# Performance work log

Hardware: AMD Instinct MI355X
Metric: run time of the kernel (lower is better)

The kernel has to match this reference:

```python
import jax, jax.numpy as jnp
import numpy as np

B = 8192
ID_DIM = 1024
LLM_DIM = 4096
IN_DIM = ID_DIM + LLM_DIM      # 5120
OUT_DIM = 2048
HID = OUT_DIM * 2              # 4096
E = 8
TOPK = 2
GATE_HID = E * 2               # 16


def setup_inputs() -> dict:
    key = jax.random.key(0)
    ks = jax.random.split(key, 12)
    s_in = 1.0 / np.sqrt(IN_DIM)
    s_hid = 1.0 / np.sqrt(HID)
    s_g = 1.0 / np.sqrt(GATE_HID)
    return {
        "id_emb": jax.random.normal(ks[0], (B, ID_DIM), jnp.float32),
        "llm_emb": jax.random.normal(ks[1], (B, LLM_DIM), jnp.float32),
        # stacked expert params
        "W1": jax.random.normal(ks[2], (E, IN_DIM, HID), jnp.float32) * s_in,
        "b1": jax.random.normal(ks[3], (E, HID), jnp.float32) * 0.01,
        "W2": jax.random.normal(ks[4], (E, HID, OUT_DIM), jnp.float32) * s_hid,
        "b2": jax.random.normal(ks[5], (E, OUT_DIM), jnp.float32) * 0.01,
        # gate params
        "gW1": jax.random.normal(ks[6], (IN_DIM, GATE_HID), jnp.float32) * s_in,
        "gb1": jax.random.normal(ks[7], (GATE_HID,), jnp.float32) * 0.01,
        "gW2": jax.random.normal(ks[8], (GATE_HID, E), jnp.float32) * s_g,
        "gb2": jax.random.normal(ks[9], (E,), jnp.float32) * 0.01,
    }


def reference(id_emb, llm_emb, W1, b1, W2, b2, gW1, gb1, gW2, gb2):
    combined = jnp.concatenate([id_emb, llm_emb], axis=-1)          # [B, IN]
    # gate: Linear -> ReLU -> Linear
    gate_logits = jax.nn.relu(combined @ gW1 + gb1) @ gW2 + gb2    # [B, E]
    topk_w, topk_i = jax.lax.top_k(gate_logits, TOPK)               # [B, K]
    topk_w = jax.nn.softmax(topk_w, axis=-1)
    # dense per-expert combine weights [B, E] (zero for non-selected experts)
    bsz = combined.shape[0]
    dense_w = jnp.zeros((bsz, E), combined.dtype).at[
        jnp.arange(bsz)[:, None], topk_i].add(topk_w)
    # dense all-experts MLP (faithful to reference: every expert on all tokens)
    h = jax.nn.relu(jnp.einsum('bi,eih->beh', combined, W1) + b1)  # [B, E, HID]
    expert_out = jnp.einsum('beh,eho->beo', h, W2) + b2            # [B, E, OUT]
    return jnp.einsum('be,beo->bo', dense_w, expert_out)           # [B, OUT]
```

## Files before the change

kernel.cpp:

```cpp
#include <hip/hip_runtime.h>
#include <hip/hip_bf16.h>
#include <hip/hip_fp16.h>

#define B_TOK 8192
#define ID_DIM 1024
#define LLM_DIM 4096
#define IN_DIM 5120
#define OUT_DIM 2048
#define HID 4096
#define NE 8
#define GH 16
#define NSLOT (2 * B_TOK)

#define NNT1 16
#define NKS1 160
#define NNT2 8
#define NKS2 128
#define MT256 72
#define GRID1B (MT256 * NNT1)
#define GRID2B (MT256 * NNT2)

typedef _Float16 f16x8 __attribute__((ext_vector_type(8)));
typedef float f32x4 __attribute__((ext_vector_type(4)));
typedef unsigned short u16;
typedef u16 u16x8 __attribute__((ext_vector_type(8)));

#define OFF_H   (1ull << 20)
#define OFF_X   (OFF_H + (size_t)NSLOT * HID * 2)
#define OFF_P1  (OFF_X + (size_t)B_TOK * IN_DIM * 2)
#define OFF_P2  (OFF_P1 + (size_t)NE * NNT1 * NKS1 * 16384)
#define REQ_WS  (OFF_P2 + (size_t)NE * NNT2 * NKS2 * 16384)
#define OFF_SLOT OFF_P1

#define INV_OFF 66560

__device__ __forceinline__ void gll16(void* lds, const void* gsrc) {
  __builtin_amdgcn_global_load_lds(
      (const __attribute__((address_space(1))) unsigned int*)gsrc,
      (__attribute__((address_space(3))) unsigned int*)lds, 16, 0, 0);
}

__global__ __launch_bounds__(256) void gate_kernel(
    const float* __restrict__ id_emb, const float* __restrict__ llm_emb,
    const float* __restrict__ gW1, const float* __restrict__ gb1,
    const float* __restrict__ gW2, const float* __restrict__ gb2,
    int* __restrict__ wsi, _Float16* __restrict__ xf16) {
  int wave = (blockIdx.x * blockDim.x + threadIdx.x) >> 6;
  int lane = threadIdx.x & 63;
  if (wave >= B_TOK) return;
  int b = wave;
  float acc[GH];
#pragma unroll
  for (int j = 0; j < GH; ++j) acc[j] = 0.f;
  for (int k = lane; k < IN_DIM; k += 64) {
    float x = (k < ID_DIM) ? id_emb[(size_t)b * ID_DIM + k]
                           : llm_emb[(size_t)b * LLM_DIM + (k - ID_DIM)];
    if (xf16) xf16[(size_t)b * IN_DIM + k] = (_Float16)x;
    const float* grow = gW1 + (size_t)k * GH;
#pragma unroll
    for (int j = 0; j < GH; ++j) acc[j] += x * grow[j];
  }
#pragma unroll
  for (int j = 0; j < GH; ++j) {
    for (int off = 32; off > 0; off >>= 1) acc[j] += __shfl_xor(acc[j], off);
  }
  if (lane == 0) {
    float logits[NE];
#pragma unroll
    for (int e = 0; e < NE; ++e) logits[e] = gb2[e];
#pragma unroll
    for (int j = 0; j < GH; ++j) {
      float hg = fmaxf(acc[j] + gb1[j], 0.f);
#pragma unroll
      for (int e = 0; e < NE; ++e) logits[e] += hg * gW2[j * NE + e];
    }
    int i0 = 0; float v0 = logits[0];
#pragma unroll
    for (int e = 1; e < NE; ++e) if (logits[e] > v0) { v0 = logits[e]; i0 = e; }
    int i1 = -1; float v1 = -1e30f;
#pragma unroll
    for (int e = 0; e < NE; ++e) if (e != i0 && logits[e] > v1) { v1 = logits[e]; i1 = e; }
    float ex = expf(v1 - v0);
    float w0 = 1.f / (1.f + ex);
    float w1 = ex / (1.f + ex);
    int* eidx = wsi + 1024;
    float* wsl = (float*)(wsi + 17408);
    eidx[b * 2] = i0; eidx[b * 2 + 1] = i1;
    wsl[b * 2] = w0; wsl[b * 2 + 1] = w1;
    atomicAdd(&wsi[i0], 1);
    atomicAdd(&wsi[i1], 1);
  }
}

__global__ void schedule_kernel(int* __restrict__ wsi) {
  if (threadIdx.x != 0 || blockIdx.x != 0) return;
  int* counts = wsi; int* cursor = wsi + 8;
  int* te = wsi + 16; int* tm = wsi + 272; int* tc = wsi + 528;
  int off = 0, t = 0;
  for (int e = 0; e < NE; ++e) {
    int c = counts[e];
    cursor[e] = off;
    int nt = (c + 255) >> 8;
    for (int i = 0; i < nt; ++i) {
      te[t] = e; tm[t] = off + i * 256;
      int rem = c - i * 256;
      tc[t] = rem < 256 ? rem : 256;
      ++t;
    }
    off += c;
  }
  for (; t < MT256; ++t) { te[t] = 0; tm[t] = 0; tc[t] = 0; }
}

__global__ __launch_bounds__(256) void scatter_kernel(int* __restrict__ wsi) {
  int s = blockIdx.x * blockDim.x + threadIdx.x;
  if (s >= NSLOT) return;
  int* cursor = wsi + 8;
  const int* eidx = wsi + 1024;
  const float* wsl = (const float*)(wsi + 17408);
  int* rows = wsi + 33792;
  float* wsorted = (float*)(wsi + 50176);
  int* inv = wsi + INV_OFF;
  int e = eidx[s];
  int pos = atomicAdd(&cursor[e], 1);
  rows[pos] = s;
  wsorted[pos] = wsl[s];
  inv[s] = pos;
}

__global__ __launch_bounds__(256) void pack_w(
    const float* __restrict__ W, _Float16* __restrict__ P,
    int N, int NNT, int NKS) {
  int ks = blockIdx.x, nt = blockIdx.y, e = blockIdx.z;
  const float* src = W + ((size_t)e * NKS * 32 + (size_t)ks * 32) * N + nt * 256;
  _Float16* dst = P + (((size_t)e * NNT + nt) * NKS + ks) * 8192;
  int t = threadIdx.x;
  int l = t & 63, q = t >> 6;
  int fr = l & 15, kg = l >> 4;
  for (int gn = q; gn < 16; gn += 4) {
    const float* s = src + (size_t)(kg * 8) * N + gn * 16 + fr;
    union { u16x8 u; _Float16 f[8]; } cv;
#pragma unroll
    for (int j = 0; j < 8; ++j) cv.f[j] = (_Float16)s[(size_t)j * N];
    *(u16x8*)(dst + gn * 512 + l * 8) = cv.u;
  }
}

#define SBAR __builtin_amdgcn_s_barrier()
#define SCHB __builtin_amdgcn_sched_barrier(0)
#define LGKM0 asm volatile("s_waitcnt lgkmcnt(0)" ::: "memory")
#define VMW(n) asm volatile("s_waitcnt vmcnt(" #n ")" ::: "memory")

#define ST_A(Aw, ks_, pa_, gm_) gll16((Aw) + (gm_) * 512, (pa_) + (size_t)(ks_) * 32)
#define ST_B(Bw, ks_, gn_) \
  gll16((Bw) + (gn_) * 512, pb + (size_t)(ks_) * 8192 + (gn_) * 512)

#define GEMM_LOOP(NKS)                                                         \
  {                                                                            \
    _Pragma("unroll") for (int kp = 0; kp < 3; ++kp) {                         \
      _Float16* Aw = smem + kp * 8192;                                         \
      _Float16* Bw = smem + 32768 + kp * 8192;                                 \
      ST_A(Aw, kp, paA, gm_a); ST_A(Aw, kp, paB, gm_b);                        \
      ST_B(Bw, kp, gnA); ST_B(Bw, kp, gnB);                                    \
    }                                                                          \
    VMW(8); SCHB; SBAR;                                                        \
    for (int k = 0; k < (NKS); ++k) {                                          \
      int rb = k & 3, wbi = (k + 3) & 3;                                       \
      _Float16* Ac = smem + rb * 8192;                                         \
      _Float16* Bc = smem + 32768 + rb * 8192;                                 \
      _Float16* Aw = smem + wbi * 8192;                                        \
      _Float16* Bw = smem + 32768 + wbi * 8192;                                \
      f16x8 a[4], b4[4];                                                       \
                                          \
      _Pragma("unroll") for (int m = 0; m < 4; ++m)                            \
          a[m] = *(const f16x8*)(Ac + (wr * 8 + m) * 512 + lane * 8);          \
      _Pragma("unroll") for (int n = 0; n < 4; ++n)                            \
          b4[n] = *(const f16x8*)(Bc + (wc * 4 + n) * 512 + lane * 8);         \
      if (k + 3 < (NKS)) {                                                     \
        ST_A(Aw, k + 3, paA, gm_a); ST_A(Aw, k + 3, paB, gm_b);                \
        ST_B(Bw, k + 3, gnA); ST_B(Bw, k + 3, gnB);                            \
      }                                                                        \
      SBAR; LGKM0; SCHB;                                                       \
      __builtin_amdgcn_s_setprio(1);                                           \
      _Pragma("unroll") for (int m = 0; m < 4; ++m)                            \
          _Pragma("unroll") for (int n = 0; n < 4; ++n)                        \
              acc[m][n] = __builtin_amdgcn_mfma_f32_16x16x32_f16(              \
                  a[m], b4[n], acc[m][n], 0, 0, 0);                            \
      __builtin_amdgcn_s_setprio(0); SCHB; SBAR;                               \
                          \
      _Pragma("unroll") for (int m = 0; m < 4; ++m)                            \
          a[m] = *(const f16x8*)(Ac + (wr * 8 + 4 + m) * 512 + lane * 8);      \
      if (k < (NKS) - 3) { VMW(8); }                                           \
      else if (k == (NKS) - 3) { VMW(4); }                                     \
      else if (k == (NKS) - 2) { VMW(0); }                                     \
      SCHB; SBAR; LGKM0; SCHB;                                                 \
      __builtin_amdgcn_s_setprio(1);                                           \
      _Pragma("unroll") for (int m = 0; m < 4; ++m)                            \
          _Pragma("unroll") for (int n = 0; n < 4; ++n)                        \
              acc[4 + m][n] = __builtin_amdgcn_mfma_f32_16x16x32_f16(          \
                  a[m], b4[n], acc[4 + m][n], 0, 0, 0);                        \
      __builtin_amdgcn_s_setprio(0); SCHB; SBAR;                               \
    }                                                                          \
  }

__global__ __launch_bounds__(512, 2) void gemm1_kernel(
    const _Float16* __restrict__ Xf, const _Float16* __restrict__ P1,
    const float* __restrict__ b1, const int* __restrict__ wsi,
    _Float16* __restrict__ hbuf) {
  __shared__ _Float16 smem[65536];
  int d = blockIdx.x;
  int orig = (d & 7) * (GRID1B >> 3) + (d >> 3);
  int tile = orig / NNT1;
  int nt = orig % NNT1;
  int cnt = (wsi + 528)[tile];
  if (cnt == 0) return;
  int e = (wsi + 16)[tile];
  int m0 = (wsi + 272)[tile];
  const int* rows = wsi + 33792;
  int n0 = nt * 256;
  int tid = threadIdx.x, lane = tid & 63, w = tid >> 6;
  int wr = w >> 2, wc = w & 3;
  int fr = lane & 15, kg = lane >> 4;

  int gm_a = wr * 8 + (w & 3);
  int gm_b = gm_a + 4;
  int gnA = w * 2, gnB = w * 2 + 1;
  int ra = gm_a * 16 + fr; ra = ra < cnt ? ra : cnt - 1;
  int rb2 = gm_b * 16 + fr; rb2 = rb2 < cnt ? rb2 : cnt - 1;
  const _Float16* paA = Xf + (size_t)(rows[m0 + ra] >> 1) * IN_DIM + kg * 8;
  const _Float16* paB = Xf + (size_t)(rows[m0 + rb2] >> 1) * IN_DIM + kg * 8;
  const _Float16* pb = P1 + ((size_t)e * NNT1 + nt) * ((size_t)NKS1 * 8192) + lane * 8;

  f32x4 acc[8][4];
#pragma unroll
  for (int m = 0; m < 8; ++m)
#pragma unroll
    for (int n = 0; n < 4; ++n) acc[m][n] = (f32x4){0.f, 0.f, 0.f, 0.f};

  GEMM_LOOP(NKS1)

  float bias_n[4];
#pragma unroll
  for (int n = 0; n < 4; ++n) bias_n[n] = b1[e * HID + n0 + wc * 64 + n * 16 + fr];

  _Float16* ep = smem;
#pragma unroll
  for (int hh = 0; hh < 2; ++hh) {
    __syncthreads();
    if (wr == hh) {
#pragma unroll
      for (int m = 0; m < 8; ++m)
#pragma unroll
        for (int n = 0; n < 4; ++n)
#pragma unroll
          for (int r2 = 0; r2 < 4; ++r2) {
            int row_loc = m * 16 + kg * 4 + r2;
            int col_loc = wc * 64 + n * 16 + fr;
            ep[row_loc * 264 + col_loc] = (_Float16)fmaxf(acc[m][n][r2] + bias_n[n], 0.f);
          }
    }
    __syncthreads();
#pragma unroll
    for (int i = 0; i < 8; ++i) {
      int chunk = i * 512 + tid;
      int row = chunk >> 5, c16 = chunk & 31;
      int r = hh * 128 + row;
      if (r < cnt)
        *(u16x8*)&hbuf[(size_t)(m0 + r) * HID + n0 + c16 * 8] =
            *(const u16x8*)&ep[row * 264 + c16 * 8];
    }
  }
}

__global__ __launch_bounds__(512, 2) void gemm2_kernel(
    const _Float16* __restrict__ hbuf, const _Float16* __restrict__ P2,
    const float* __restrict__ b2, const int* __restrict__ wsi,
    float* __restrict__ slotbuf) {
  __shared__ _Float16 smem[65536];
  int d = blockIdx.x;
  int orig = (d & 7) * (GRID2B >> 3) + (d >> 3);
  int tile = orig / NNT2;
  int nt = orig % NNT2;
  int cnt = (wsi + 528)[tile];
  if (cnt == 0) return;
  int e = (wsi + 16)[tile];
  int m0 = (wsi + 272)[tile];
  const float* wsorted = (const float*)(wsi + 50176);
  int n0 = nt * 256;
  int tid = threadIdx.x, lane = tid & 63, w = tid >> 6;
  int wr = w >> 2, wc = w & 3;
  int fr = lane & 15, kg = lane >> 4;

  int gm_a = wr * 8 + (w & 3);
  int gm_b = gm_a + 4;
  int gnA = w * 2, gnB = w * 2 + 1;
  int ra = gm_a * 16 + fr; ra = ra < cnt ? ra : cnt - 1;
  int rb2 = gm_b * 16 + fr; rb2 = rb2 < cnt ? rb2 : cnt - 1;
  const _Float16* paA = hbuf + (size_t)(m0 + ra) * HID + kg * 8;
  const _Float16* paB = hbuf + (size_t)(m0 + rb2) * HID + kg * 8;
  const _Float16* pb = P2 + ((size_t)e * NNT2 + nt) * ((size_t)NKS2 * 8192) + lane * 8;

  f32x4 acc[8][4];
#pragma unroll
  for (int m = 0; m < 8; ++m)
#pragma unroll
    for (int n = 0; n < 4; ++n) acc[m][n] = (f32x4){0.f, 0.f, 0.f, 0.f};

  GEMM_LOOP(NKS2)

  float bias_n[4];
#pragma unroll
  for (int n = 0; n < 4; ++n) bias_n[n] = b2[e * OUT_DIM + n0 + wc * 64 + n * 16 + fr];

#pragma unroll
  for (int m = 0; m < 8; ++m) {
#pragma unroll
    for (int r2 = 0; r2 < 4; ++r2) {
      int r = wr * 128 + m * 16 + kg * 4 + r2;
      if (r < cnt) {
        float wgt = wsorted[m0 + r];
        float* orow = slotbuf + (size_t)(m0 + r) * OUT_DIM + n0;
#pragma unroll
        for (int n = 0; n < 4; ++n)
          orow[wc * 64 + n * 16 + fr] = (acc[m][n][r2] + bias_n[n]) * wgt;
      }
    }
  }
}

__global__ __launch_bounds__(256) void combine_kernel(
    const float* __restrict__ slotbuf, const int* __restrict__ wsi,
    float* __restrict__ out) {
  int idx = blockIdx.x * 256 + threadIdx.x;
  int b = idx >> 9, c4 = (idx & 511) * 4;
  const int* inv = wsi + INV_OFF;
  int p0 = inv[b * 2], p1 = inv[b * 2 + 1];
  float4 a = *(const float4*)&slotbuf[(size_t)p0 * OUT_DIM + c4];
  float4 c = *(const float4*)&slotbuf[(size_t)p1 * OUT_DIM + c4];
  float4 o; o.x = a.x + c.x; o.y = a.y + c.y; o.z = a.z + c.z; o.w = a.w + c.w;
  *(float4*)&out[(size_t)b * OUT_DIM + c4] = o;
}

#define FB_MAX_TILES 136
__global__ void schedule_fb(int* __restrict__ wsi) {
  if (threadIdx.x != 0 || blockIdx.x != 0) return;
  int* counts = wsi; int* cursor = wsi + 8;
  int* te = wsi + 16; int* tm = wsi + 272; int* tc = wsi + 528;
  int off = 0, t = 0;
  for (int e = 0; e < NE; ++e) {
    int c = counts[e];
    cursor[e] = off;
    int nt = (c + 127) >> 7;
    for (int i = 0; i < nt; ++i) {
      te[t] = e; tm[t] = off + i * 128;
      int rem = c - i * 128;
      tc[t] = rem < 128 ? rem : 128;
      ++t;
    }
    off += c;
  }
  for (; t < FB_MAX_TILES; ++t) { te[t] = 0; tm[t] = 0; tc[t] = 0; }
}

__global__ __launch_bounds__(256, 2) void gemm1_fb(
    const float* __restrict__ id_emb, const float* __restrict__ llm_emb,
    const float* __restrict__ W1, const float* __restrict__ b1,
    const int* __restrict__ wsi, _Float16* __restrict__ h) {
  const int* te = wsi + 16; const int* tm = wsi + 272; const int* tc = wsi + 528;
  const int* rows = wsi + 33792;
  int tile = blockIdx.x;
  int cnt = tc[tile];
  if (cnt == 0) return;
  int e = te[tile], m0 = tm[tile];
  int n0 = blockIdx.y * 128;
  const float* Wb = W1 + (size_t)e * IN_DIM * HID;
  __shared__ _Float16 As[128][40];
  __shared__ _Float16 Bs[128][40];
  int tid = threadIdx.x;
  int lane = tid & 63, w = tid >> 6;
  int wr = w >> 1, wc = w & 1;
  int fr = lane & 15, kg = lane >> 4;
  f32x4 acc[4][4];
#pragma unroll
  for (int m = 0; m < 4; ++m)
#pragma unroll
    for (int n = 0; n < 4; ++n) acc[m][n] = (f32x4){0.f, 0.f, 0.f, 0.f};
  int a_ks = (tid & 3) * 8;
  int a_r = tid >> 2;
  int brow[2];
#pragma unroll
  for (int i = 0; i < 2; ++i) {
    int r = a_r + i * 64;
    brow[i] = (r < cnt) ? (rows[m0 + r] >> 1) : -1;
  }
  int b_c = tid & 127, b_kq = tid >> 7;
  for (int kt = 0; kt < IN_DIM; kt += 32) {
#pragma unroll
    for (int i = 0; i < 2; ++i) {
      int r = a_r + i * 64;
      float v[8];
      if (brow[i] >= 0) {
        int k = kt + a_ks;
        const float* src = (k < ID_DIM)
            ? (id_emb + (size_t)brow[i] * ID_DIM + k)
            : (llm_emb + (size_t)brow[i] * LLM_DIM + (k - ID_DIM));
        float4 v0 = *(const float4*)src;
        float4 v1 = *(const float4*)(src + 4);
        v[0] = v0.x; v[1] = v0.y; v[2] = v0.z; v[3] = v0.w;
        v[4] = v1.x; v[5] = v1.y; v[6] = v1.z; v[7] = v1.w;
      } else {
#pragma unroll
        for (int j = 0; j < 8; ++j) v[j] = 0.f;
      }
      union { u16x8 u; _Float16 f[8]; } cv;
#pragma unroll
      for (int j = 0; j < 8; ++j) cv.f[j] = (_Float16)v[j];
      *reinterpret_cast<u16x8*>(&As[r][a_ks]) = cv.u;
    }
#pragma unroll
    for (int i = 0; i < 2; ++i) {
      int kc = b_kq + i * 2;
      int k0 = kt + kc * 8;
      union { u16x8 u; _Float16 f[8]; } cv;
#pragma unroll
      for (int j = 0; j < 8; ++j)
        cv.f[j] = (_Float16)Wb[(size_t)(k0 + j) * HID + n0 + b_c];
      *reinterpret_cast<u16x8*>(&Bs[b_c][kc * 8]) = cv.u;
    }
    __syncthreads();
    f16x8 af[4], bf[4];
#pragma unroll
    for (int m = 0; m < 4; ++m)
      af[m] = *reinterpret_cast<const f16x8*>(&As[wr * 64 + m * 16 + fr][kg * 8]);
#pragma unroll
    for (int n = 0; n < 4; ++n)
      bf[n] = *reinterpret_cast<const f16x8*>(&Bs[wc * 64 + n * 16 + fr][kg * 8]);
#pragma unroll
    for (int m = 0; m < 4; ++m)
#pragma unroll
      for (int n = 0; n < 4; ++n)
        acc[m][n] = __builtin_amdgcn_mfma_f32_16x16x32_f16(af[m], bf[n], acc[m][n], 0, 0, 0);
    __syncthreads();
  }
#pragma unroll
  for (int m = 0; m < 4; ++m) {
    int rbv = wr * 64 + m * 16 + kg * 4;
#pragma unroll
    for (int n = 0; n < 4; ++n) {
      int col = n0 + wc * 64 + n * 16 + fr;
      float bias = b1[e * HID + col];
#pragma unroll
      for (int r2 = 0; r2 < 4; ++r2) {
        int r = rbv + r2;
        if (r < cnt) {
          float v = fmaxf(acc[m][n][r2] + bias, 0.f);
          h[(size_t)(m0 + r) * HID + col] = (_Float16)v;
        }
      }
    }
  }
}

__global__ __launch_bounds__(256, 2) void gemm2_fb(
    const _Float16* __restrict__ h, const float* __restrict__ W2,
    const float* __restrict__ b2, const int* __restrict__ wsi,
    float* __restrict__ out) {
  const int* te = wsi + 16; const int* tm = wsi + 272; const int* tc = wsi + 528;
  const int* rows = wsi + 33792;
  const float* wsorted = (const float*)(wsi + 50176);
  int tile = blockIdx.x;
  int cnt = tc[tile];
  if (cnt == 0) return;
  int e = te[tile], m0 = tm[tile];
  int n0 = blockIdx.y * 128;
  const float* Wb = W2 + (size_t)e * HID * OUT_DIM;
  __shared__ _Float16 As[128][40];
  __shared__ _Float16 Bs[128][40];
  int tid = threadIdx.x;
  int lane = tid & 63, w = tid >> 6;
  int wr = w >> 1, wc = w & 1;
  int fr = lane & 15, kg = lane >> 4;
  f32x4 acc[4][4];
#pragma unroll
  for (int m = 0; m < 4; ++m)
#pragma unroll
    for (int n = 0; n < 4; ++n) acc[m][n] = (f32x4){0.f, 0.f, 0.f, 0.f};
  int a_ks = (tid & 3) * 8;
  int a_r = tid >> 2;
  int b_c = tid & 127, b_kq = tid >> 7;
  for (int kt = 0; kt < HID; kt += 32) {
#pragma unroll
    for (int i = 0; i < 2; ++i) {
      int r = a_r + i * 64;
      u16x8 v;
      if (r < cnt) {
        v = *reinterpret_cast<const u16x8*>(&h[(size_t)(m0 + r) * HID + kt + a_ks]);
      } else {
        v = (u16x8){0, 0, 0, 0, 0, 0, 0, 0};
      }
      *reinterpret_cast<u16x8*>(&As[r][a_ks]) = v;
    }
#pragma unroll
    for (int i = 0; i < 2; ++i) {
      int kc = b_kq + i * 2;
      int k0 = kt + kc * 8;
      union { u16x8 u; _Float16 f[8]; } cv;
#pragma unroll
      for (int j = 0; j < 8; ++j)
        cv.f[j] = (_Float16)Wb[(size_t)(k0 + j) * OUT_DIM + n0 + b_c];
      *reinterpret_cast<u16x8*>(&Bs[b_c][kc * 8]) = cv.u;
    }
    __syncthreads();
    f16x8 af[4], bf[4];
#pragma unroll
    for (int m = 0; m < 4; ++m)
      af[m] = *reinterpret_cast<const f16x8*>(&As[wr * 64 + m * 16 + fr][kg * 8]);
#pragma unroll
    for (int n = 0; n < 4; ++n)
      bf[n] = *reinterpret_cast<const f16x8*>(&Bs[wc * 64 + n * 16 + fr][kg * 8]);
#pragma unroll
    for (int m = 0; m < 4; ++m)
#pragma unroll
      for (int n = 0; n < 4; ++n)
        acc[m][n] = __builtin_amdgcn_mfma_f32_16x16x32_f16(af[m], bf[n], acc[m][n], 0, 0, 0);
    __syncthreads();
  }
#pragma unroll
  for (int m = 0; m < 4; ++m) {
    int rbv = wr * 64 + m * 16 + kg * 4;
#pragma unroll
    for (int n = 0; n < 4; ++n) {
      int col = n0 + wc * 64 + n * 16 + fr;
      float bias = b2[e * OUT_DIM + col];
#pragma unroll
      for (int r2 = 0; r2 < 4; ++r2) {
        int r = rbv + r2;
        if (r < cnt) {
          int slot = rows[m0 + r];
          int btok = slot >> 1;
          float wgt = wsorted[m0 + r];
          atomicAdd(&out[(size_t)btok * OUT_DIM + col], (acc[m][n][r2] + bias) * wgt);
        }
      }
    }
  }
}

extern "C" void kernel_launch(void* const* d_in, const int* in_sizes, int n_in,
                              void* d_out, int out_size, void* d_ws, size_t ws_size,
                              hipStream_t stream) {
  const float* id_emb  = (const float*)d_in[0];
  const float* llm_emb = (const float*)d_in[1];
  const float* W1  = (const float*)d_in[2];
  const float* b1  = (const float*)d_in[3];
  const float* W2  = (const float*)d_in[4];
  const float* b2  = (const float*)d_in[5];
  const float* gW1 = (const float*)d_in[6];
  const float* gb1 = (const float*)d_in[7];
  const float* gW2 = (const float*)d_in[8];
  const float* gb2 = (const float*)d_in[9];
  float* out = (float*)d_out;
  int* wsi = (int*)d_ws;
  _Float16* h = (_Float16*)((char*)d_ws + OFF_H);
  bool fast = ws_size >= REQ_WS;

  hipMemsetAsync(d_ws, 0, 4096, stream);

  if (fast) {
    _Float16* xf = (_Float16*)((char*)d_ws + OFF_X);
    _Float16* p1 = (_Float16*)((char*)d_ws + OFF_P1);
    _Float16* p2 = (_Float16*)((char*)d_ws + OFF_P2);
    float* slotbuf = (float*)((char*)d_ws + OFF_SLOT);
    gate_kernel<<<B_TOK / 4, 256, 0, stream>>>(id_emb, llm_emb, gW1, gb1, gW2, gb2, wsi, xf);
    schedule_kernel<<<1, 64, 0, stream>>>(wsi);
    scatter_kernel<<<NSLOT / 256, 256, 0, stream>>>(wsi);
    pack_w<<<dim3(NKS1, NNT1, NE), 256, 0, stream>>>(W1, p1, HID, NNT1, NKS1);
    pack_w<<<dim3(NKS2, NNT2, NE), 256, 0, stream>>>(W2, p2, OUT_DIM, NNT2, NKS2);
    gemm1_kernel<<<GRID1B, 512, 0, stream>>>(xf, p1, b1, wsi, h);
    gemm2_kernel<<<GRID2B, 512, 0, stream>>>(h, p2, b2, wsi, slotbuf);
    combine_kernel<<<(B_TOK * OUT_DIM / 4) / 256, 256, 0, stream>>>(slotbuf, wsi, out);
  } else {
    hipMemsetAsync(d_out, 0, (size_t)B_TOK * OUT_DIM * sizeof(float), stream);
    gate_kernel<<<B_TOK / 4, 256, 0, stream>>>(id_emb, llm_emb, gW1, gb1, gW2, gb2, wsi, nullptr);
    schedule_fb<<<1, 64, 0, stream>>>(wsi);
    scatter_kernel<<<NSLOT / 256, 256, 0, stream>>>(wsi);
    gemm1_fb<<<dim3(FB_MAX_TILES, 32), 256, 0, stream>>>(id_emb, llm_emb, W1, b1, wsi, h);
    gemm2_fb<<<dim3(FB_MAX_TILES, 16), 256, 0, stream>>>(h, W2, b2, wsi, out);
  }
}
```

Measured before the change: 1.933 ms.

## Software-pipeline LDS fragment reads across k-steps with register double buffering

Replaces the GEMM main loop with a two-way unrolled pipeline. The next k-step's A0/B fragments are read from LDS while the current MFMAs issue, using ping-pong register sets. This cuts the loop from four barriers and two explicit lgkmcnt waits per k-step to one barrier. The goal is to hide LDS read latency behind MFMA work. It costs more VGPRs at 2 blocks per CU, and the single barrier means the 4-buffer ring must still prevent overwriting a stage that other waves are reading.

After: 1.856 ms. 1.04x faster.

```diff
diff --git a/kernel.cpp b/kernel.cpp
--- a/kernel.cpp
+++ b/kernel.cpp
@@ -148,59 +148,59 @@
 
 #define SBAR __builtin_amdgcn_s_barrier()
 #define SCHB __builtin_amdgcn_sched_barrier(0)
-#define LGKM0 asm volatile("s_waitcnt lgkmcnt(0)" ::: "memory")
 #define VMW(n) asm volatile("s_waitcnt vmcnt(" #n ")" ::: "memory")
 
 #define ST_A(Aw, ks_, pa_, gm_) gll16((Aw) + (gm_) * 512, (pa_) + (size_t)(ks_) * 32)
 #define ST_B(Bw, ks_, gn_) \
   gll16((Bw) + (gn_) * 512, pb + (size_t)(ks_) * 8192 + (gn_) * 512)
 
-#define GEMM_LOOP(NKS)                                                         \
-  {                                                                            \
-    _Pragma("unroll") for (int kp = 0; kp < 3; ++kp) {                         \
-      _Float16* Aw = smem + kp * 8192;                                         \
-      _Float16* Bw = smem + 32768 + kp * 8192;                                 \
-      ST_A(Aw, kp, paA, gm_a); ST_A(Aw, kp, paB, gm_b);                        \
-      ST_B(Bw, kp, gnA); ST_B(Bw, kp, gnB);                                    \
-    }                                                                          \
-    VMW(8); SCHB; SBAR;                                                        \
-    for (int k = 0; k < (NKS); ++k) {                                          \
-      int rb = k & 3, wbi = (k + 3) & 3;                                       \
-      _Float16* Ac = smem + rb * 8192;                                         \
-      _Float16* Bc = smem + 32768 + rb * 8192;                                 \
-      _Float16* Aw = smem + wbi * 8192;                                        \
-      _Float16* Bw = smem + 32768 + wbi * 8192;                                \
-      f16x8 a[4], b4[4];                                                       \
-                                          \
-      _Pragma("unroll") for (int m = 0; m < 4; ++m)                            \
-          a[m] = *(const f16x8*)(Ac + (wr * 8 + m) * 512 + lane * 8);          \
-      _Pragma("unroll") for (int n = 0; n < 4; ++n)                            \
-          b4[n] = *(const f16x8*)(Bc + (wc * 4 + n) * 512 + lane * 8);         \
-      if (k + 3 < (NKS)) {                                                     \
-        ST_A(Aw, k + 3, paA, gm_a); ST_A(Aw, k + 3, paB, gm_b);                \
-        ST_B(Bw, k + 3, gnA); ST_B(Bw, k + 3, gnB);                            \
-      }                                                                        \
-      SBAR; LGKM0; SCHB;                                                       \
-      __builtin_amdgcn_s_setprio(1);                                           \
-      _Pragma("unroll") for (int m = 0; m < 4; ++m)                            \
-          _Pragma("unroll") for (int n = 0; n < 4; ++n)                        \
-              acc[m][n] = __builtin_amdgcn_mfma_f32_16x16x32_f16(              \
-                  a[m], b4[n], acc[m][n], 0, 0, 0);                            \
-      __builtin_amdgcn_s_setprio(0); SCHB; SBAR;                               \
-                          \
-      _Pragma("unroll") for (int m = 0; m < 4; ++m)                            \
-          a[m] = *(const f16x8*)(Ac + (wr * 8 + 4 + m) * 512 + lane * 8);      \
-      if (k < (NKS) - 3) { VMW(8); }                                           \
-      else if (k == (NKS) - 3) { VMW(4); }                                     \
-      else if (k == (NKS) - 2) { VMW(0); }                                     \
-      SCHB; SBAR; LGKM0; SCHB;                                                 \
-      __builtin_amdgcn_s_setprio(1);                                           \
-      _Pragma("unroll") for (int m = 0; m < 4; ++m)                            \
-          _Pragma("unroll") for (int n = 0; n < 4; ++n)                        \
-              acc[4 + m][n] = __builtin_amdgcn_mfma_f32_16x16x32_f16(          \
-                  a[m], b4[n], acc[4 + m][n], 0, 0, 0);                        \
-      __builtin_amdgcn_s_setprio(0); SCHB; SBAR;                               \
-    }                                                                          \
+#define STAGE4(kt)                                                   \
+  { _Float16* Aw = smem + ((kt) & 3) * 8192;                         \
+    _Float16* Bw = smem + 32768 + ((kt) & 3) * 8192;                 \
+    ST_A(Aw, kt, paA, gm_a); ST_A(Aw, kt, paB, gm_b);                \
+    ST_B(Bw, kt, gnA); ST_B(Bw, kt, gnB); }
+
+#define READ_A0B(A0s, Bs, Acp, Bcp)                                   \
+  _Pragma("unroll") for (int m = 0; m < 4; ++m)                       \
+      A0s[m] = *(const f16x8*)((Acp) + (wr * 8 + m) * 512 + lane * 8);\
+  _Pragma("unroll") for (int n = 0; n < 4; ++n)                       \
+      Bs[n] = *(const f16x8*)((Bcp) + (wc * 4 + n) * 512 + lane * 8);
+
+#define READ_A1(Acp)                                                  \
+  _Pragma("unroll") for (int m = 0; m < 4; ++m)                       \
+      A1[m] = *(const f16x8*)((Acp) + (wr * 8 + 4 + m) * 512 + lane * 8);
+
+#define MFMA_CL(As, Bs, MO)                                           \
+  __builtin_amdgcn_s_setprio(1);                                      \
+  _Pragma("unroll") for (int m = 0; m < 4; ++m)                       \
+      _Pragma("unroll") for (int n = 0; n < 4; ++n)                   \
+          acc[(MO) + m][n] = __builtin_amdgcn_mfma_f32_16x16x32_f16(  \
+              As[m], Bs[n], acc[(MO) + m][n], 0, 0, 0);               \
+  __builtin_amdgcn_s_setprio(0);
+
+#define PIPE_ITER(A0c, Bc_, A0n, Bn_, k, NKS)                         \
+  { if ((k) < (NKS) - 2) { VMW(4); } else { VMW(0); }                 \
+    SCHB; SBAR;                                                       \
+    if ((k) + 3 < (NKS)) STAGE4((k) + 3);                             \
+    _Float16* Acur = smem + ((k) & 3) * 8192;                         \
+    READ_A1(Acur); SCHB;                                              \
+    MFMA_CL(A0c, Bc_, 0)                                              \
+    if ((k) + 1 < (NKS)) {                                            \
+      _Float16* An_ = smem + (((k) + 1) & 3) * 8192;                  \
+      _Float16* Bn2 = smem + 32768 + (((k) + 1) & 3) * 8192;          \
+      READ_A0B(A0n, Bn_, An_, Bn2)                                    \
+    }                                                                 \
+    SCHB;                                                             \
+    MFMA_CL(A1, Bc_, 4) }
+
+#define GEMM_PIPE(NKS)                                                \
+  f16x8 A0x[4], Bx[4], A0y[4], By[4], A1[4];                          \
+  STAGE4(0) STAGE4(1) STAGE4(2)                                       \
+  VMW(8); SCHB; SBAR;                                                 \
+  READ_A0B(A0x, Bx, smem, smem + 32768)                               \
+  for (int k = 0; k < (NKS); k += 2) {                                \
+    PIPE_ITER(A0x, Bx, A0y, By, k, (NKS))                             \
+    PIPE_ITER(A0y, By, A0x, Bx, (k + 1), (NKS))                       \
   }
 
 __global__ __launch_bounds__(512, 2) void gemm1_kernel(
@@ -237,7 +237,7 @@
 #pragma unroll
     for (int n = 0; n < 4; ++n) acc[m][n] = (f32x4){0.f, 0.f, 0.f, 0.f};
 
-  GEMM_LOOP(NKS1)
+  GEMM_PIPE(NKS1)
 
   float bias_n[4];
 #pragma unroll
@@ -306,7 +306,7 @@
 #pragma unroll
     for (int n = 0; n < 4; ++n) acc[m][n] = (f32x4){0.f, 0.f, 0.f, 0.f};
 
-  GEMM_LOOP(NKS2)
+  GEMM_PIPE(NKS2)
 
   float bias_n[4];
 #pragma unroll
```
